# Kernel optimization log

Hardware: AMD Instinct MI355X
Metric: run time of the kernel (lower is better)

The kernel has to match this reference:

```python
import jax, jax.numpy as jnp
import numpy as np
import math

B, S, DIM = 2, 2048, 1024
H, D = 16, 64  # num_head, head_dim; H*D == DIM

def setup_inputs() -> dict:
    key = jax.random.key(0)
    ks = jax.random.split(key, 10)
    s = 0.02
    return {
        "X": jax.random.normal(ks[0], (B, S, DIM), dtype=jnp.float32),
        "mask": jnp.ones((B, S), dtype=jnp.float32),
        "Wq": jax.random.normal(ks[1], (DIM, H * D), dtype=jnp.float32) * s,
        "bq": jnp.zeros((H * D,), dtype=jnp.float32),
        "Wk": jax.random.normal(ks[2], (DIM, H * D), dtype=jnp.float32) * s,
        "bk": jnp.zeros((H * D,), dtype=jnp.float32),
        "Wv": jax.random.normal(ks[3], (DIM, H * D), dtype=jnp.float32) * s,
        "bv": jnp.zeros((H * D,), dtype=jnp.float32),
        "Wo": jax.random.normal(ks[4], (H * D, DIM), dtype=jnp.float32) * s,
        "bo": jnp.zeros((DIM,), dtype=jnp.float32),
    }

def _split_heads(x):
    # [B, S, H*D] -> [B, H, S, D]
    b, s, _ = x.shape
    return x.reshape(b, s, H, D).transpose(0, 2, 1, 3)

def reference(X, mask, Wq, bq, Wk, bk, Wv, bv, Wo, bo):
    Q = _split_heads(X @ Wq + bq)
    K = _split_heads(X @ Wk + bk)
    V = _split_heads(X @ Wv + bv)
    # scaled dot-product attention with additive mask penalty
    dot = jnp.einsum('bhqd,bhkd->bhqk', Q, K) / math.sqrt(D)
    dot = dot - 1e6 * (1.0 - mask[:, None, None, :])
    attn = jax.nn.softmax(dot, axis=-1)
    ctx = jnp.einsum('bhqk,bhkd->bhqd', attn, V)
    # combine heads: [B, H, S, D] -> [B, S, H*D]
    ctx = ctx.transpose(0, 2, 1, 3).reshape(B, S, H * D)
    return ctx @ Wo + bo
```

## Files before the change

kernel.cpp:

```cpp
#include <hip/hip_runtime.h>
#include <cstdint>
#include <cstddef>

typedef __attribute__((ext_vector_type(8))) _Float16 f16x8;
typedef __attribute__((ext_vector_type(4))) _Float16 f16x4;
typedef __attribute__((ext_vector_type(4))) float f32x4;

#define MFMA_16x16x32(a, b, c) __builtin_amdgcn_mfma_f32_16x16x32_f16((a), (b), (c), 0, 0, 0)

static constexpr int kB = 2, kS = 2048, kDim = 1024, kH = 16, kD = 64;
static constexpr int kM = kB * kS;
static constexpr float kQScale = 0.125f * 1.44269504088896340736f;

__global__ void cvt_f32_to_f16(const float* __restrict__ in, _Float16* __restrict__ out, int n8) {
  int i = blockIdx.x * blockDim.x + threadIdx.x;
  if (i >= n8) return;
  const float4* p = (const float4*)in + (size_t)i * 2;
  float4 a = p[0], b = p[1];
  f16x8 h;
  h[0] = (_Float16)a.x; h[1] = (_Float16)a.y; h[2] = (_Float16)a.z; h[3] = (_Float16)a.w;
  h[4] = (_Float16)b.x; h[5] = (_Float16)b.y; h[6] = (_Float16)b.z; h[7] = (_Float16)b.w;
  ((f16x8*)out)[i] = h;
}

__global__ void transpose_cvt_w(const float* __restrict__ w0, const float* __restrict__ w1,
                                const float* __restrict__ w2, const float* __restrict__ w3,
                                _Float16* __restrict__ o0, _Float16* __restrict__ o1,
                                _Float16* __restrict__ o2, _Float16* __restrict__ o3) {
  const float* w; _Float16* o;
  switch (blockIdx.z) {
    case 0: w = w0; o = o0; break;
    case 1: w = w1; o = o1; break;
    case 2: w = w2; o = o2; break;
    default: w = w3; o = o3; break;
  }
  __shared__ alignas(16) _Float16 tile[64][72];
  const int kt = blockIdx.x * 64;
  const int nt = blockIdx.y * 64;
  const int tr = threadIdx.x >> 4;
  const int tc = threadIdx.x & 15;
#pragma unroll
  for (int rr = 0; rr < 4; ++rr) {
    int r = rr * 16 + tr;
    float4 v = *(const float4*)&w[(size_t)(kt + r) * kDim + nt + tc * 4];
    f16x4 hv;
    hv[0] = (_Float16)v.x; hv[1] = (_Float16)v.y; hv[2] = (_Float16)v.z; hv[3] = (_Float16)v.w;
    *(f16x4*)&tile[r][tc * 4] = hv;
  }
  __syncthreads();
#pragma unroll
  for (int rr = 0; rr < 4; ++rr) {
    int nl = rr * 16 + tr;
    f16x4 hv;
    hv[0] = tile[tc * 4 + 0][nl];
    hv[1] = tile[tc * 4 + 1][nl];
    hv[2] = tile[tc * 4 + 2][nl];
    hv[3] = tile[tc * 4 + 3][nl];
    *(f16x4*)&o[(size_t)(nt + nl) * kDim + kt + tc * 4] = hv;
  }
}

__global__ void mask_penalty(const float* __restrict__ mask, float* __restrict__ pen, int n) {
  int i = blockIdx.x * blockDim.x + threadIdx.x;
  if (i < n) pen[i] = -1.0e6f * (1.0f - mask[i]) * 1.44269504088896340736f;
}

__global__ __launch_bounds__(256, 2) void gemm_qkv(
    const _Float16* __restrict__ A,
    const _Float16* __restrict__ wt0, const _Float16* __restrict__ wt1, const _Float16* __restrict__ wt2,
    const float* __restrict__ bias0, const float* __restrict__ bias1, const float* __restrict__ bias2,
    _Float16* __restrict__ oq, _Float16* __restrict__ ok, _Float16* __restrict__ ov) {
  const _Float16* Bt; const float* bias; _Float16* out;
  switch (blockIdx.z) {
    case 0: Bt = wt0; bias = bias0; out = oq; break;
    case 1: Bt = wt1; bias = bias1; out = ok; break;
    default: Bt = wt2; bias = bias2; out = ov; break;
  }
  __shared__ alignas(16) _Float16 As[128 * 72];
  __shared__ alignas(16) _Float16 Bs[128 * 72];
  const int tid = threadIdx.x;
  const int lane = tid & 63;
  const int wave = tid >> 6;
  const int wm = wave & 1, wn = wave >> 1;
  const int l15 = lane & 15, quad = lane >> 4;
  const int m0 = blockIdx.x * 128, n0 = blockIdx.y * 128;

  f32x4 acc[4][4] = {};

  for (int k0 = 0; k0 < kDim; k0 += 64) {
    __syncthreads();
#pragma unroll
    for (int i = 0; i < 4; ++i) {
      int c = tid + 256 * i;
      int row = c >> 3, kc = (c & 7) * 8;
      *(f16x8*)&As[row * 72 + kc] = *(const f16x8*)&A[(size_t)(m0 + row) * kDim + k0 + kc];
      *(f16x8*)&Bs[row * 72 + kc] = *(const f16x8*)&Bt[(size_t)(n0 + row) * kDim + k0 + kc];
    }
    __syncthreads();
#pragma unroll
    for (int kk = 0; kk < 2; ++kk) {
      f16x8 af[4], bf[4];
#pragma unroll
      for (int t = 0; t < 4; ++t) af[t] = *(const f16x8*)&As[(wm * 64 + t * 16 + l15) * 72 + kk * 32 + quad * 8];
#pragma unroll
      for (int t = 0; t < 4; ++t) bf[t] = *(const f16x8*)&Bs[(wn * 64 + t * 16 + l15) * 72 + kk * 32 + quad * 8];
#pragma unroll
      for (int i = 0; i < 4; ++i)
#pragma unroll
        for (int j = 0; j < 4; ++j)
          acc[i][j] = MFMA_16x16x32(af[i], bf[j], acc[i][j]);
    }
  }

  const int mbase = m0 + wm * 64 + quad * 4;
  const int nbase = n0 + wn * 64 + l15;
  if (blockIdx.z == 2) {
#pragma unroll
    for (int j = 0; j < 4; ++j) {
      int n = nbase + j * 16;
      float bv = bias[n];
      int h = n >> 6, d = n & 63;
#pragma unroll
      for (int i = 0; i < 4; ++i) {
        int m = mbase + i * 16;
        int b = m >> 11, s = m & (kS - 1);
        f16x4 hv;
#pragma unroll
        for (int r = 0; r < 4; ++r) hv[r] = (_Float16)(acc[i][j][r] + bv);
        *(f16x4*)&out[((size_t)((b * kH + h) * kD + d)) * kS + s] = hv;
      }
    }
  } else {
    const float osc = (blockIdx.z == 0) ? kQScale : 1.0f;
#pragma unroll
    for (int j = 0; j < 4; ++j) {
      int n = nbase + j * 16;
      float bv = bias[n];
      int h = n >> 6, d = n & 63;
#pragma unroll
      for (int i = 0; i < 4; ++i) {
        int mrow = mbase + i * 16;
#pragma unroll
        for (int r = 0; r < 4; ++r) {
          int m = mrow + r;
          int b = m >> 11, s = m & (kS - 1);
          out[(size_t)(((b * kH + h) * kS) + s) * kD + d] = (_Float16)((acc[i][j][r] + bv) * osc);
        }
      }
    }
  }
}

__global__ __launch_bounds__(256, 2) void attn(
    const _Float16* __restrict__ Q, const _Float16* __restrict__ K,
    const _Float16* __restrict__ V, const float* __restrict__ pen2,
    _Float16* __restrict__ ctx) {
  const int bh = blockIdx.y;
  const int b = bh >> 4;
  const int q0 = blockIdx.x * 128;
  const int tid = threadIdx.x, lane = tid & 63, wave = tid >> 6;
  const int l15 = lane & 15, quad = lane >> 4;

  __shared__ alignas(16) _Float16 Ks[128 * 72];
  __shared__ alignas(16) _Float16 Vs[64 * 136];
  __shared__ alignas(16) _Float16 Pt[4][32 * 136];
  __shared__ alignas(16) float pens[128];

  const _Float16* Qh = Q + (size_t)bh * kS * kD;
  const _Float16* Kh = K + (size_t)bh * kS * kD;
  const _Float16* Vh = V + (size_t)bh * kS * kD;

  f16x8 qf[2][2];
#pragma unroll
  for (int t = 0; t < 2; ++t) {
    int qrow = q0 + wave * 32 + t * 16 + l15;
#pragma unroll
    for (int kk = 0; kk < 2; ++kk)
      qf[t][kk] = *(const f16x8*)&Qh[(size_t)qrow * kD + kk * 32 + quad * 8];
  }

  f32x4 o_acc[2][4] = {};
  float l_part[2] = {0.0f, 0.0f};

  for (int kb = 0; kb < kS; kb += 128) {
    __syncthreads();
#pragma unroll
    for (int i = 0; i < 4; ++i) {
      int c = tid + 256 * i;
      int row = c >> 3, dc = (c & 7) * 8;
      *(f16x8*)&Ks[row * 72 + dc] = *(const f16x8*)&Kh[(size_t)(kb + row) * kD + dc];
    }
#pragma unroll
    for (int i = 0; i < 4; ++i) {
      int c = tid + 256 * i;
      int row = c >> 4, sc8 = (c & 15) * 8;
      *(f16x8*)&Vs[row * 136 + sc8] = *(const f16x8*)&Vh[(size_t)row * kS + kb + sc8];
    }
    if (tid < 128) pens[tid] = pen2[b * kS + kb + tid];
    __syncthreads();

    f32x4 s[2][8] = {};
#pragma unroll
    for (int kk = 0; kk < 2; ++kk)
#pragma unroll
      for (int colt = 0; colt < 8; ++colt) {
        f16x8 kf = *(const f16x8*)&Ks[(colt * 16 + l15) * 72 + kk * 32 + quad * 8];
        s[0][colt] = MFMA_16x16x32(kf, qf[0][kk], s[0][colt]);
        s[1][colt] = MFMA_16x16x32(kf, qf[1][kk], s[1][colt]);
      }

#pragma unroll
    for (int t = 0; t < 2; ++t) {
#pragma unroll
      for (int colt = 0; colt < 8; ++colt) {
        f32x4 pn = *(const f32x4*)&pens[colt * 16 + quad * 4];
        f16x4 ph;
#pragma unroll
        for (int r = 0; r < 4; ++r) {
          float pv = __builtin_exp2f(s[t][colt][r] + pn[r]);
          l_part[t] += pv;
          ph[r] = (_Float16)pv;
        }
        *(f16x4*)&Pt[wave][(t * 16 + l15) * 136 + colt * 16 + quad * 4] = ph;
      }
    }

#pragma unroll
    for (int ks = 0; ks < 4; ++ks) {
      f16x8 pf0 = *(const f16x8*)&Pt[wave][(l15) * 136 + ks * 32 + quad * 8];
      f16x8 pf1 = *(const f16x8*)&Pt[wave][(16 + l15) * 136 + ks * 32 + quad * 8];
#pragma unroll
      for (int c = 0; c < 4; ++c) {
        f16x8 vf = *(const f16x8*)&Vs[(c * 16 + l15) * 136 + ks * 32 + quad * 8];
        o_acc[0][c] = MFMA_16x16x32(vf, pf0, o_acc[0][c]);
        o_acc[1][c] = MFMA_16x16x32(vf, pf1, o_acc[1][c]);
      }
    }
  }

  const int h = bh & 15;
#pragma unroll
  for (int t = 0; t < 2; ++t) {
    float lsum = l_part[t];
    lsum += __shfl_xor(lsum, 16, 64);
    lsum += __shfl_xor(lsum, 32, 64);
    float inv = 1.0f / lsum;
    int q = q0 + wave * 32 + t * 16 + l15;
#pragma unroll
    for (int c = 0; c < 4; ++c) {
      f16x4 oh;
#pragma unroll
      for (int r = 0; r < 4; ++r) oh[r] = (_Float16)(o_acc[t][c][r] * inv);
      *(f16x4*)&ctx[((size_t)(b * kS + q)) * kDim + h * kD + c * 16 + quad * 4] = oh;
    }
  }
}

__global__ __launch_bounds__(256, 2) void gemm_out(
    const _Float16* __restrict__ A, const _Float16* __restrict__ Bt,
    const float* __restrict__ bias, float* __restrict__ out) {
  __shared__ alignas(16) _Float16 As[128 * 72];
  __shared__ alignas(16) _Float16 Bs[128 * 72];
  const int tid = threadIdx.x;
  const int lane = tid & 63;
  const int wave = tid >> 6;
  const int wm = wave & 1, wn = wave >> 1;
  const int l15 = lane & 15, quad = lane >> 4;
  const int m0 = blockIdx.x * 128, n0 = blockIdx.y * 128;

  f32x4 acc[4][4] = {};

  for (int k0 = 0; k0 < kDim; k0 += 64) {
    __syncthreads();
#pragma unroll
    for (int i = 0; i < 4; ++i) {
      int c = tid + 256 * i;
      int row = c >> 3, kc = (c & 7) * 8;
      *(f16x8*)&As[row * 72 + kc] = *(const f16x8*)&A[(size_t)(m0 + row) * kDim + k0 + kc];
      *(f16x8*)&Bs[row * 72 + kc] = *(const f16x8*)&Bt[(size_t)(n0 + row) * kDim + k0 + kc];
    }
    __syncthreads();
#pragma unroll
    for (int kk = 0; kk < 2; ++kk) {
      f16x8 af[4], bf[4];
#pragma unroll
      for (int t = 0; t < 4; ++t) af[t] = *(const f16x8*)&As[(wm * 64 + t * 16 + l15) * 72 + kk * 32 + quad * 8];
#pragma unroll
      for (int t = 0; t < 4; ++t) bf[t] = *(const f16x8*)&Bs[(wn * 64 + t * 16 + l15) * 72 + kk * 32 + quad * 8];
#pragma unroll
      for (int i = 0; i < 4; ++i)
#pragma unroll
        for (int j = 0; j < 4; ++j)
          acc[i][j] = MFMA_16x16x32(af[i], bf[j], acc[i][j]);
    }
  }

  const int mbase = m0 + wm * 64 + quad * 4;
  const int nbase = n0 + wn * 64 + l15;
#pragma unroll
  for (int j = 0; j < 4; ++j) {
    int n = nbase + j * 16;
    float bv = bias[n];
#pragma unroll
    for (int i = 0; i < 4; ++i) {
      int mrow = mbase + i * 16;
#pragma unroll
      for (int r = 0; r < 4; ++r)
        out[(size_t)(mrow + r) * kDim + n] = acc[i][j][r] + bv;
    }
  }
}

extern "C" void kernel_launch(void* const* d_in, const int* in_sizes, int n_in,
                              void* d_out, int out_size, void* d_ws, size_t ws_size,
                              hipStream_t stream) {
  (void)in_sizes; (void)n_in; (void)out_size; (void)ws_size;
  const float* X    = (const float*)d_in[0];
  const float* mask = (const float*)d_in[1];
  const float* Wq   = (const float*)d_in[2];
  const float* bq   = (const float*)d_in[3];
  const float* Wk   = (const float*)d_in[4];
  const float* bk   = (const float*)d_in[5];
  const float* Wv   = (const float*)d_in[6];
  const float* bv   = (const float*)d_in[7];
  const float* Wo   = (const float*)d_in[8];
  const float* bo   = (const float*)d_in[9];
  float* out = (float*)d_out;

  char* ws = (char*)d_ws;
  _Float16* Xh   = (_Float16*)(ws);
  _Float16* Wqt  = (_Float16*)(ws + ((size_t)8  << 20));
  _Float16* Wkt  = (_Float16*)(ws + ((size_t)10 << 20));
  _Float16* Wvt  = (_Float16*)(ws + ((size_t)12 << 20));
  _Float16* Wot  = (_Float16*)(ws + ((size_t)14 << 20));
  _Float16* Qh   = (_Float16*)(ws + ((size_t)16 << 20));
  _Float16* Kh   = (_Float16*)(ws + ((size_t)24 << 20));
  _Float16* Vh   = (_Float16*)(ws + ((size_t)32 << 20));
  _Float16* Ch   = (_Float16*)(ws + ((size_t)40 << 20));
  float*    pen2 = (float*)   (ws + ((size_t)48 << 20));

  cvt_f32_to_f16<<<dim3(kM * kDim / 8 / 256), dim3(256), 0, stream>>>(X, Xh, kM * kDim / 8);
  transpose_cvt_w<<<dim3(16, 16, 4), dim3(256), 0, stream>>>(Wq, Wk, Wv, Wo, Wqt, Wkt, Wvt, Wot);
  mask_penalty<<<dim3(16), dim3(256), 0, stream>>>(mask, pen2, kB * kS);
  gemm_qkv<<<dim3(32, 8, 3), dim3(256), 0, stream>>>(Xh, Wqt, Wkt, Wvt, bq, bk, bv, Qh, Kh, Vh);
  attn<<<dim3(16, 32), dim3(256), 0, stream>>>(Qh, Kh, Vh, pen2, Ch);
  gemm_out<<<dim3(32, 8), dim3(256), 0, stream>>>(Ch, Wot, bo, out);
}
```

Measured before the change: 219.7 us.

## Double-buffer LDS tiles with register prefetch in QKV and output GEMMs

Both projection GEMMs now keep two LDS buffers and prefetch the next K tile from global memory into registers while MFMAs run on the current tile. The prefetched tile is written to the other buffer afterwards, so each iteration needs one barrier instead of two. The goal is to hide global load latency behind compute. In exchange, LDS per block doubles to about 72 KB and the staging registers add pressure, which could reduce occupancy below the two blocks per CU that the launch bounds request.

```diff
diff --git a/kernel.cpp b/kernel.cpp
--- a/kernel.cpp
+++ b/kernel.cpp
@@ -76,8 +76,8 @@
     case 1: Bt = wt1; bias = bias1; out = ok; break;
     default: Bt = wt2; bias = bias2; out = ov; break;
   }
-  __shared__ alignas(16) _Float16 As[128 * 72];
-  __shared__ alignas(16) _Float16 Bs[128 * 72];
+  __shared__ alignas(16) _Float16 As[2][128 * 72];
+  __shared__ alignas(16) _Float16 Bs[2][128 * 72];
   const int tid = threadIdx.x;
   const int lane = tid & 63;
   const int wave = tid >> 6;
@@ -85,30 +85,57 @@
   const int l15 = lane & 15, quad = lane >> 4;
   const int m0 = blockIdx.x * 128, n0 = blockIdx.y * 128;
 
+  const int srow = tid >> 3;
+  const int skc = (tid & 7) * 8;
+
   f32x4 acc[4][4] = {};
-
-  for (int k0 = 0; k0 < kDim; k0 += 64) {
-    __syncthreads();
-#pragma unroll
-    for (int i = 0; i < 4; ++i) {
-      int c = tid + 256 * i;
-      int row = c >> 3, kc = (c & 7) * 8;
-      *(f16x8*)&As[row * 72 + kc] = *(const f16x8*)&A[(size_t)(m0 + row) * kDim + k0 + kc];
-      *(f16x8*)&Bs[row * 72 + kc] = *(const f16x8*)&Bt[(size_t)(n0 + row) * kDim + k0 + kc];
+  f16x8 ra[4], rb[4];
+
+#pragma unroll
+  for (int i = 0; i < 4; ++i) {
+    int row = srow + 32 * i;
+    ra[i] = *(const f16x8*)&A[(size_t)(m0 + row) * kDim + skc];
+    rb[i] = *(const f16x8*)&Bt[(size_t)(n0 + row) * kDim + skc];
+  }
+#pragma unroll
+  for (int i = 0; i < 4; ++i) {
+    int row = srow + 32 * i;
+    *(f16x8*)&As[0][row * 72 + skc] = ra[i];
+    *(f16x8*)&Bs[0][row * 72 + skc] = rb[i];
+  }
+
+  for (int kt = 0; kt < 16; ++kt) {
+    const int cur = kt & 1;
+    if (kt + 1 < 16) {
+      int k0 = (kt + 1) * 64;
+#pragma unroll
+      for (int i = 0; i < 4; ++i) {
+        int row = srow + 32 * i;
+        ra[i] = *(const f16x8*)&A[(size_t)(m0 + row) * kDim + k0 + skc];
+        rb[i] = *(const f16x8*)&Bt[(size_t)(n0 + row) * kDim + k0 + skc];
+      }
     }
     __syncthreads();
 #pragma unroll
     for (int kk = 0; kk < 2; ++kk) {
       f16x8 af[4], bf[4];
 #pragma unroll
-      for (int t = 0; t < 4; ++t) af[t] = *(const f16x8*)&As[(wm * 64 + t * 16 + l15) * 72 + kk * 32 + quad * 8];
-#pragma unroll
-      for (int t = 0; t < 4; ++t) bf[t] = *(const f16x8*)&Bs[(wn * 64 + t * 16 + l15) * 72 + kk * 32 + quad * 8];
+      for (int t = 0; t < 4; ++t) af[t] = *(const f16x8*)&As[cur][(wm * 64 + t * 16 + l15) * 72 + kk * 32 + quad * 8];
+#pragma unroll
+      for (int t = 0; t < 4; ++t) bf[t] = *(const f16x8*)&Bs[cur][(wn * 64 + t * 16 + l15) * 72 + kk * 32 + quad * 8];
 #pragma unroll
       for (int i = 0; i < 4; ++i)
 #pragma unroll
         for (int j = 0; j < 4; ++j)
           acc[i][j] = MFMA_16x16x32(af[i], bf[j], acc[i][j]);
+    }
+    if (kt + 1 < 16) {
+#pragma unroll
+      for (int i = 0; i < 4; ++i) {
+        int row = srow + 32 * i;
+        *(f16x8*)&As[cur ^ 1][row * 72 + skc] = ra[i];
+        *(f16x8*)&Bs[cur ^ 1][row * 72 + skc] = rb[i];
+      }
     }
   }
 
@@ -259,8 +286,8 @@
 __global__ __launch_bounds__(256, 2) void gemm_out(
     const _Float16* __restrict__ A, const _Float16* __restrict__ Bt,
     const float* __restrict__ bias, float* __restrict__ out) {
-  __shared__ alignas(16) _Float16 As[128 * 72];
-  __shared__ alignas(16) _Float16 Bs[128 * 72];
+  __shared__ alignas(16) _Float16 As[2][128 * 72];
+  __shared__ alignas(16) _Float16 Bs[2][128 * 72];
   const int tid = threadIdx.x;
   const int lane = tid & 63;
   const int wave = tid >> 6;
@@ -268,30 +295,57 @@
   const int l15 = lane & 15, quad = lane >> 4;
   const int m0 = blockIdx.x * 128, n0 = blockIdx.y * 128;
 
+  const int srow = tid >> 3;
+  const int skc = (tid & 7) * 8;
+
   f32x4 acc[4][4] = {};
-
-  for (int k0 = 0; k0 < kDim; k0 += 64) {
-    __syncthreads();
-#pragma unroll
-    for (int i = 0; i < 4; ++i) {
-      int c = tid + 256 * i;
-      int row = c >> 3, kc = (c & 7) * 8;
-      *(f16x8*)&As[row * 72 + kc] = *(const f16x8*)&A[(size_t)(m0 + row) * kDim + k0 + kc];
-      *(f16x8*)&Bs[row * 72 + kc] = *(const f16x8*)&Bt[(size_t)(n0 + row) * kDim + k0 + kc];
+  f16x8 ra[4], rb[4];
+
+#pragma unroll
+  for (int i = 0; i < 4; ++i) {
+    int row = srow + 32 * i;
+    ra[i] = *(const f16x8*)&A[(size_t)(m0 + row) * kDim + skc];
+    rb[i] = *(const f16x8*)&Bt[(size_t)(n0 + row) * kDim + skc];
+  }
+#pragma unroll
+  for (int i = 0; i < 4; ++i) {
+    int row = srow + 32 * i;
+    *(f16x8*)&As[0][row * 72 + skc] = ra[i];
+    *(f16x8*)&Bs[0][row * 72 + skc] = rb[i];
+  }
+
+  for (int kt = 0; kt < 16; ++kt) {
+    const int cur = kt & 1;
+    if (kt + 1 < 16) {
+      int k0 = (kt + 1) * 64;
+#pragma unroll
+      for (int i = 0; i < 4; ++i) {
+        int row = srow + 32 * i;
+        ra[i] = *(const f16x8*)&A[(size_t)(m0 + row) * kDim + k0 + skc];
+        rb[i] = *(const f16x8*)&Bt[(size_t)(n0 + row) * kDim + k0 + skc];
+      }
     }
     __syncthreads();
 #pragma unroll
     for (int kk = 0; kk < 2; ++kk) {
       f16x8 af[4], bf[4];
 #pragma unroll
-      for (int t = 0; t < 4; ++t) af[t] = *(const f16x8*)&As[(wm * 64 + t * 16 + l15) * 72 + kk * 32 + quad * 8];
-#pragma unroll
-      for (int t = 0; t < 4; ++t) bf[t] = *(const f16x8*)&Bs[(wn * 64 + t * 16 + l15) * 72 + kk * 32 + quad * 8];
+      for (int t = 0; t < 4; ++t) af[t] = *(const f16x8*)&As[cur][(wm * 64 + t * 16 + l15) * 72 + kk * 32 + quad * 8];
+#pragma unroll
+      for (int t = 0; t < 4; ++t) bf[t] = *(const f16x8*)&Bs[cur][(wn * 64 + t * 16 + l15) * 72 + kk * 32 + quad * 8];
 #pragma unroll
       for (int i = 0; i < 4; ++i)
 #pragma unroll
         for (int j = 0; j < 4; ++j)
           acc[i][j] = MFMA_16x16x32(af[i], bf[j], acc[i][j]);
+    }
+    if (kt + 1 < 16) {
+#pragma unroll
+      for (int i = 0; i < 4; ++i) {
+        int row = srow + 32 * i;
+        *(f16x8*)&As[cur ^ 1][row * 72 + skc] = ra[i];
+        *(f16x8*)&Bs[cur ^ 1][row * 72 + skc] = rb[i];
+      }
     }
   }
 
```

Result: faster. 215.1 us (-2.1%).
